# Optimization experiments

Measured on AMD Instinct MI355X. Metric: run time of the kernel, lower is better.

Reference implementation:

```python
import jax, jax.numpy as jnp
import numpy as np

B, L, H = 2, 4096, 1024
ED, N, R, K = 2048, 16, 64, 4


def setup_inputs() -> dict:
    key = jax.random.key(0)
    ks = jax.random.split(key, 8)
    w = lambda i, shape, s=0.02: jax.random.normal(ks[i], shape, jnp.float32) * s
    # dt bias initialized like Mamba: inv-softplus of dt ~ logU(1e-3, 1e-1)
    dt = jnp.exp(jax.random.uniform(ks[7], (ED,)) * (np.log(0.1) - np.log(0.001)) + np.log(0.001))
    dt = jnp.clip(dt, 1e-4)
    inv_dt = dt + jnp.log(-jnp.expm1(-dt))
    A = jnp.broadcast_to(jnp.arange(1, N + 1, dtype=jnp.float32), (ED, N))
    return dict(
        x=jax.random.normal(ks[0], (B, L, H), jnp.float32),
        in_proj_w=w(1, (2 * ED, H)),
        conv_w=w(2, (ED, K), 0.2),
        conv_b=jnp.zeros((ED,), jnp.float32),
        x_proj_w=w(3, (R + 2 * N, ED)),
        dt_w=w(4, (ED, R), 64 ** -0.5),
        dt_b=inv_dt,
        A_log=jnp.log(A),
        D=jnp.ones((ED,), jnp.float32),
        out_proj_w=w(5, (H, ED)),
    )


def reference(x, in_proj_w, conv_w, conv_b, x_proj_w, dt_w, dt_b, A_log, D, out_proj_w):
    Bq, Lq, Hq = x.shape
    EDq, Kq = conv_w.shape
    Rq = dt_w.shape[1]
    Nq = A_log.shape[1]

    # in_proj -> [B, L, 2*ED]; chunk into hidden_states and gate
    xz = jnp.einsum('blh,eh->ble', x, in_proj_w)
    hs, gate = jnp.split(xz, 2, axis=-1)

    # causal depthwise conv1d along L (padding K-1 on the left), then SiLU
    hs_pad = jnp.pad(hs, ((0, 0), (Kq - 1, 0), (0, 0)))  # [B, L+K-1, ED]
    conv = conv_b
    for k in range(Kq):  # K=4, fixed small loop
        conv = conv + hs_pad[:, k:k + Lq, :] * conv_w[:, k]
    hs = jax.nn.silu(conv)  # [B, L, ED]

    # x_proj -> split into dt (rank R), B (N), C (N)
    ssm = jnp.einsum('ble,pe->blp', hs, x_proj_w)
    dtr, Bm, Cm = jnp.split(ssm, [Rq, Rq + Nq], axis=-1)

    # dt_proj + softplus (delta_softplus=True with delta_bias)
    delta = jax.nn.softplus(jnp.einsum('blr,er->ble', dtr, dt_w) + dt_b)  # [B,L,ED]

    A = -jnp.exp(A_log)  # [ED, N]

    # selective scan: h_t = exp(delta_t*A)*h_{t-1} + delta_t*B_t*u_t ; y_t = <h_t, C_t>
    def step(h, inp):
        d_t, B_t, C_t, u_t = inp  # [B,ED], [B,N], [B,N], [B,ED]
        dA = jnp.exp(d_t[..., None] * A)                      # [B,ED,N]
        h = dA * h + (d_t * u_t)[..., None] * B_t[:, None, :]  # [B,ED,N]
        y = jnp.einsum('ben,bn->be', h, C_t)                   # [B,ED]
        return h, y

    h0 = jnp.zeros((Bq, EDq, Nq), x.dtype)
    xs = (jnp.moveaxis(delta, 1, 0), jnp.moveaxis(Bm, 1, 0),
          jnp.moveaxis(Cm, 1, 0), jnp.moveaxis(hs, 1, 0))
    _, ys = jax.lax.scan(step, h0, xs)  # ys: [L, B, ED]

    y = jnp.moveaxis(ys, 0, 1) + hs * D      # skip term D*u
    y = y * jax.nn.silu(gate)                # gated output
    return jnp.einsum('ble,he->blh', y, out_proj_w)
```

## Files before the change

### kernel.cpp

```cpp
#include <hip/hip_runtime.h>


typedef float f32x4 __attribute__((ext_vector_type(4)));
typedef short short8 __attribute__((ext_vector_type(8)));
typedef unsigned short u16;

#define DEV __device__ __forceinline__

DEV float bf2f(u16 u) {
  union { unsigned int i; float f; } v; v.i = ((unsigned int)u) << 16; return v.f;
}
DEV u16 f2bf(float f) {
  union { float f; unsigned int i; } v; v.f = f;
  return (u16)((v.i + 0x7fffu + ((v.i >> 16) & 1u)) >> 16);
}

DEV void gload_lds16(const void* g, void* l) {
  __builtin_amdgcn_global_load_lds(
      (const __attribute__((address_space(1))) unsigned int*)g,
      (__attribute__((address_space(3))) unsigned int*)l, 16, 0, 0);
}

DEV void mfma_bf16(f32x4& d, short8 a, short8 b) {
  asm("v_mfma_f32_16x16x32_bf16 %0, %1, %2, %0" : "+v"(d) : "v"(a), "v"(b));
}

template <int N> DEV void wait_vmcnt() {
  if constexpr (N == 0)      asm volatile("s_waitcnt vmcnt(0)" ::: "memory");
  else if constexpr (N == 1) asm volatile("s_waitcnt vmcnt(1)" ::: "memory");
  else if constexpr (N == 2) asm volatile("s_waitcnt vmcnt(2)" ::: "memory");
  else if constexpr (N == 4) asm volatile("s_waitcnt vmcnt(4)" ::: "memory");
  else if constexpr (N == 6) asm volatile("s_waitcnt vmcnt(6)" ::: "memory");
  else                       asm volatile("s_waitcnt vmcnt(8)" ::: "memory");
}

#define SYNC_PRE() do { __builtin_amdgcn_s_barrier(); \
  asm volatile("s_waitcnt lgkmcnt(0)" ::: "memory"); \
  __builtin_amdgcn_sched_barrier(0); \
  __builtin_amdgcn_s_setprio(1); } while (0)
#define SYNC_POST() do { __builtin_amdgcn_s_setprio(0); \
  __builtin_amdgcn_sched_barrier(0); \
  __builtin_amdgcn_s_barrier(); } while (0)

template <int EPI>
__global__ __launch_bounds__(512, 2) void gemm256_kernel(
    const u16* __restrict__ A, const u16* __restrict__ Bw,
    int M, int N, int Kd,
    float* __restrict__ o_f32, u16* __restrict__ o_b16a, u16* __restrict__ o_b16b)
{
  __shared__ u16 lds[65536];
  const int tid  = threadIdx.x;
  const int wave = tid >> 6;
  const int lane = tid & 63;
  const int row  = lane & 15;
  const int g    = lane >> 4;
  const int wr   = wave >> 2;
  const int wc   = wave & 3;

  const int nbx = N >> 8;
  const int nwg = gridDim.x;
  const int cpx = nwg >> 3;
  const int swzb = (blockIdx.x & 7) * cpx + (blockIdx.x >> 3);
  const int bx = swzb % nbx, by = swzb / nbx;
  const int rowBase = by * 256, colBase = bx * 256;

  auto STAGE = [&](int isB, int h, int kt) {
    const u16* src = isB ? Bw : A;
    const int baseRow = (isB ? colBase : rowBase) + h * 128;
    const int ldsbase = (kt & 1) * 32768 + isB * 16384 + h * 8192;
    const int kk = kt * 64;
#pragma unroll
    for (int q = 0; q < 2; ++q) {
      int c = q * 512 + tid;
      int r = c >> 3;
      int qc = (c & 7) ^ (r & 7);
      gload_lds16(src + (size_t)(baseRow + r) * Kd + kk + qc * 8,
                  (void*)(lds + ldsbase + (q * 512 + wave * 64) * 8));
    }
  };

  f32x4 acc[8][4];
#pragma unroll
  for (int i = 0; i < 8; ++i)
#pragma unroll
    for (int j = 0; j < 4; ++j) acc[i][j] = (f32x4){0.f, 0.f, 0.f, 0.f};

  short8 rA[8], rB0[4], rB1[4];

#define LDA(PAR, MH) do { \
  _Pragma("unroll") for (int mi = 0; mi < 4; ++mi) \
  _Pragma("unroll") for (int ks = 0; ks < 2; ++ks) \
    rA[mi*2+ks] = *(const short8*)(lds + (PAR)*32768 + wr*8192 \
        + ((MH)*64 + mi*16 + row)*64 + (((ks*4 + g) ^ (row & 7))*8)); \
} while (0)

#define LDB(PAR, NH, RB) do { \
  _Pragma("unroll") for (int ni = 0; ni < 2; ++ni) \
  _Pragma("unroll") for (int ks = 0; ks < 2; ++ks) \
    (RB)[ni*2+ks] = *(const short8*)(lds + (PAR)*32768 + 16384 + (wc>>1)*8192 \
        + (((wc&1)*64 + (NH)*32 + ni*16 + row)*64) + (((ks*4 + g) ^ (row & 7))*8)); \
} while (0)

#define QUAD(MH, NH, RB) do { \
  _Pragma("unroll") for (int mi = 0; mi < 4; ++mi) \
  _Pragma("unroll") for (int ni = 0; ni < 2; ++ni) \
  _Pragma("unroll") for (int ks = 0; ks < 2; ++ks) \
    mfma_bf16(acc[(MH)*4+mi][(NH)*2+ni], rA[mi*2+ks], (RB)[ni*2+ks]); \
} while (0)

  const int nkt = Kd >> 6;
  const int niters = nkt >> 1;

  STAGE(0, 0, 0); STAGE(0, 1, 0); STAGE(1, 0, 0); STAGE(1, 1, 0);
  STAGE(1, 0, 1); STAGE(1, 1, 1); STAGE(0, 0, 1);
  wait_vmcnt<6>();
  __builtin_amdgcn_s_barrier();

  for (int i = 0; i < niters; ++i) {
    const int kt0 = 2 * i, kt1 = 2 * i + 1;
    const bool pf = (i + 1 < niters);
    LDA(0, 0); LDB(0, 0, rB0); STAGE(0, 1, kt1);
    SYNC_PRE(); QUAD(0, 0, rB0); SYNC_POST();
    LDB(0, 1, rB1);
    SYNC_PRE(); QUAD(0, 1, rB1); SYNC_POST();
    LDA(0, 1);
    if (pf) { STAGE(1, 0, kt0 + 2); STAGE(1, 1, kt0 + 2); }
    SYNC_PRE(); QUAD(1, 0, rB0); SYNC_POST();
    if (pf) { STAGE(0, 0, kt0 + 2); wait_vmcnt<6>(); } else { wait_vmcnt<0>(); }
    SYNC_PRE(); QUAD(1, 1, rB1); SYNC_POST();
    LDA(1, 0); LDB(1, 0, rB0);
    if (pf) STAGE(0, 1, kt0 + 2);
    SYNC_PRE(); QUAD(0, 0, rB0); SYNC_POST();
    LDB(1, 1, rB1);
    SYNC_PRE(); QUAD(0, 1, rB1); SYNC_POST();
    LDA(1, 1);
    if (pf) { STAGE(1, 0, kt1 + 2); STAGE(1, 1, kt1 + 2); }
    SYNC_PRE(); QUAD(1, 0, rB0); SYNC_POST();
    if (pf) { STAGE(0, 0, kt1 + 2); wait_vmcnt<6>(); } else { wait_vmcnt<0>(); }
    SYNC_PRE(); QUAD(1, 1, rB1); SYNC_POST();
  }
#undef LDA
#undef LDB
#undef QUAD

#pragma unroll
  for (int mf = 0; mf < 8; ++mf) {
    const int growb = rowBase + wr * 128 + (mf >> 2) * 64 + (mf & 3) * 16 + g * 4;
#pragma unroll
    for (int nf = 0; nf < 4; ++nf) {
      const int gcol = colBase + wc * 64 + (nf >> 1) * 32 + (nf & 1) * 16 + row;
#pragma unroll
      for (int r4 = 0; r4 < 4; ++r4) {
        const int grow = growb + r4;
        float v = acc[mf][nf][r4];
        if constexpr (EPI == 0) {
          o_f32[(size_t)grow * N + gcol] = v;
        } else {
          if (gcol < 2048) o_b16a[(size_t)grow * 2048 + gcol] = f2bf(v);
          else             o_b16b[(size_t)grow * 2048 + (gcol - 2048)] = f2bf(v);
        }
      }
    }
  }
}

template <int BM, int BN, int WM, int WN, int EPI>
__global__ __launch_bounds__(256) void gemm_bt_kernel(
    const u16* __restrict__ A, const u16* __restrict__ Bw,
    int M, int N, int Kd,
    float* __restrict__ o_f32, u16* __restrict__ o_b16a,
    u16* __restrict__ o_b16b, const float* __restrict__ bias,
    float* __restrict__ oB, float* __restrict__ oC)
{
  constexpr int MFR = BM / WM / 16;
  constexpr int NFR = BN / WN / 16;
  constexpr int TA = BM * 4;
  constexpr int TB = BN * 4;
  constexpr int TILE = (BM + BN) * 32;
  constexpr int LA3 = (TA > 192) ? ((TA - 193) / 256 + 1) : 0;
  constexpr int LB3 = (TB > 192) ? ((TB - 193) / 256 + 1) : 0;
  constexpr int LPS = LA3 + LB3;
  __shared__ u16 lds[TILE * 3];

  const int tid  = threadIdx.x;
  const int wave = tid >> 6;
  const int lane = tid & 63;
  const int row  = lane & 15;
  const int g    = lane >> 4;
  const int swz  = g ^ ((row >> 1) & 3);
  const int rowBase = blockIdx.y * BM;
  const int colBase = blockIdx.x * BN;
  const int WROW = (wave / WN) * (BM / WM);
  const int WCOL = (wave % WN) * (BN / WN);

  auto stage = [&](int kt, int bufbase) {
    const int kk = kt * 32;
#pragma unroll
    for (int c0 = 0; c0 < TA; c0 += 256) {
      int ch = c0 + tid;
      if (ch < TA) {
        int r = ch >> 2;
        int gs = (ch & 3) ^ ((r >> 1) & 3);
        gload_lds16(A + (size_t)(rowBase + r) * Kd + kk + gs * 8,
                    (void*)(lds + bufbase + (c0 + wave * 64) * 8));
      }
    }
#pragma unroll
    for (int c0 = 0; c0 < TB; c0 += 256) {
      int ch = c0 + tid;
      if (ch < TB) {
        int r = ch >> 2;
        int gs = (ch & 3) ^ ((r >> 1) & 3);
        gload_lds16(Bw + (size_t)(colBase + r) * Kd + kk + gs * 8,
                    (void*)(lds + bufbase + BM * 32 + (c0 + wave * 64) * 8));
      }
    }
  };

  f32x4 acc[MFR][NFR];
#pragma unroll
  for (int i = 0; i < MFR; ++i)
#pragma unroll
    for (int j = 0; j < NFR; ++j) acc[i][j] = (f32x4){0.f, 0.f, 0.f, 0.f};

  const int nt = Kd / 32;
  stage(0, 0);
  stage(1, TILE);
  int cur = 0;
  for (int t = 0; t < nt; ++t) {
    if (t + 2 < nt) {
      int b2 = cur + 2; if (b2 >= 3) b2 -= 3;
      stage(t + 2, b2 * TILE);
      wait_vmcnt<2 * LPS>();
    } else if (t + 1 < nt) {
      wait_vmcnt<LPS>();
    } else {
      wait_vmcnt<0>();
    }
    __builtin_amdgcn_sched_barrier(0);
    __builtin_amdgcn_s_barrier();
    __builtin_amdgcn_sched_barrier(0);
    const u16* lb = lds + cur * TILE;
    short8 af[MFR], bfr[NFR];
#pragma unroll
    for (int mi = 0; mi < MFR; ++mi)
      af[mi] = *(const short8*)(lb + (WROW + mi * 16 + row) * 32 + swz * 8);
#pragma unroll
    for (int ni = 0; ni < NFR; ++ni)
      bfr[ni] = *(const short8*)(lb + BM * 32 + (WCOL + ni * 16 + row) * 32 + swz * 8);
#pragma unroll
    for (int mi = 0; mi < MFR; ++mi)
#pragma unroll
      for (int ni = 0; ni < NFR; ++ni)
        mfma_bf16(acc[mi][ni], af[mi], bfr[ni]);
    __builtin_amdgcn_sched_barrier(0);
    __builtin_amdgcn_s_barrier();
    cur += 1; if (cur >= 3) cur -= 3;
  }

#pragma unroll
  for (int mi = 0; mi < MFR; ++mi) {
#pragma unroll
    for (int ni = 0; ni < NFR; ++ni) {
      const int gcol = colBase + WCOL + ni * 16 + row;
#pragma unroll
      for (int r = 0; r < 4; ++r) {
        const int grow = rowBase + WROW + mi * 16 + g * 4 + r;
        float v = acc[mi][ni][r];
        if constexpr (EPI == 0) {
          o_f32[(size_t)grow * N + gcol] = v;
        } else if constexpr (EPI == 1) {
          if (gcol < 2048) o_b16a[(size_t)grow * 2048 + gcol] = f2bf(v);
          else             o_b16b[(size_t)grow * 2048 + (gcol - 2048)] = f2bf(v);
        } else if constexpr (EPI == 2) {
          if (gcol < 64)      o_b16a[(size_t)grow * 64 + gcol] = f2bf(v);
          else if (gcol < 80) oB[(size_t)grow * 16 + (gcol - 64)] = v;
          else                oC[(size_t)grow * 16 + (gcol - 80)] = v;
        } else {
          float x = v + bias[gcol];
          o_f32[(size_t)grow * N + gcol] = (x > 20.f) ? x : __logf(1.f + __expf(x));
        }
      }
    }
  }
}

__global__ __launch_bounds__(256) void cvt_bf16_kernel(
    const float* __restrict__ in, u16* __restrict__ out, int n8)
{
  int i = blockIdx.x * 256 + threadIdx.x;
  if (i >= n8) return;
  const float4* p = (const float4*)(in + (size_t)i * 8);
  float4 a = p[0], b = p[1];
  float v[8] = {a.x, a.y, a.z, a.w, b.x, b.y, b.z, b.w};
  unsigned o[4];
#pragma unroll
  for (int q = 0; q < 4; ++q)
    o[q] = (unsigned)f2bf(v[2 * q]) | ((unsigned)f2bf(v[2 * q + 1]) << 16);
  *(uint4*)(out + (size_t)i * 8) = make_uint4(o[0], o[1], o[2], o[3]);
}

__global__ __launch_bounds__(256) void conv_silu_kernel(
    const u16* __restrict__ hsraw, const float* __restrict__ cw,
    const float* __restrict__ cb, u16* __restrict__ hsb)
{
  int idx = blockIdx.x * 256 + threadIdx.x;
  int e0 = (idx & 255) * 8;
  int t  = (idx >> 8) & 4095;
  int b  = idx >> 20;
  float acc[8];
  float wv[4][8];
#pragma unroll
  for (int j = 0; j < 8; ++j) acc[j] = cb[e0 + j];
#pragma unroll
  for (int k = 0; k < 4; ++k)
#pragma unroll
    for (int j = 0; j < 8; ++j) wv[k][j] = cw[(e0 + j) * 4 + k];
#pragma unroll
  for (int k = 0; k < 4; ++k) {
    int tt = t - 3 + k;
    if (tt < 0) continue;
    uint4 v4 = *(const uint4*)(hsraw + ((size_t)(b * 4096 + tt)) * 2048 + e0);
    unsigned arr[4] = {v4.x, v4.y, v4.z, v4.w};
#pragma unroll
    for (int q = 0; q < 4; ++q) {
      acc[2 * q]     += wv[k][2 * q]     * bf2f((u16)(arr[q] & 0xffffu));
      acc[2 * q + 1] += wv[k][2 * q + 1] * bf2f((u16)(arr[q] >> 16));
    }
  }
  unsigned o[4];
#pragma unroll
  for (int q = 0; q < 4; ++q) {
    float a0 = acc[2 * q], a1 = acc[2 * q + 1];
    a0 = a0 / (1.f + __expf(-a0));
    a1 = a1 / (1.f + __expf(-a1));
    o[q] = (unsigned)f2bf(a0) | ((unsigned)f2bf(a1) << 16);
  }
  *(uint4*)(hsb + ((size_t)(b * 4096 + t)) * 2048 + e0) = make_uint4(o[0], o[1], o[2], o[3]);
}

__global__ __launch_bounds__(256) void scan_phase1(
    const float* __restrict__ delta, const u16* __restrict__ hsb,
    const float* __restrict__ Bb, const float* __restrict__ alog,
    float* __restrict__ h_end, float* __restrict__ Ssum)
{
  __shared__ __align__(16) float Bs[64 * 16];
  const int tid = threadIdx.x;
  const int e = blockIdx.x * 256 + tid;
  const int c = blockIdx.y;
  const int b = blockIdx.z;
  const int t0 = c * 64;
  {
    const float* src = Bb + ((size_t)(b * 4096 + t0)) * 16;
#pragma unroll
    for (int k = 0; k < 4; ++k) Bs[tid + k * 256] = src[tid + k * 256];
  }
  float An[16];
  {
    const float4* ap = (const float4*)(alog + e * 16);
#pragma unroll
    for (int q = 0; q < 4; ++q) {
      float4 v = ap[q];
      An[4*q+0] = -__expf(v.x); An[4*q+1] = -__expf(v.y);
      An[4*q+2] = -__expf(v.z); An[4*q+3] = -__expf(v.w);
    }
  }
  __syncthreads();
  float h[16];
#pragma unroll
  for (int n = 0; n < 16; ++n) h[n] = 0.f;
  float sumd = 0.f;
  size_t base = ((size_t)(b * 4096 + t0)) * 2048 + e;
  float dd = delta[base];
  float uu = bf2f(hsb[base]);
  for (int j = 0; j < 64; ++j) {
    int jn = (j < 63) ? j + 1 : 63;
    float d_nxt = delta[base + (size_t)jn * 2048];
    float u_nxt = bf2f(hsb[base + (size_t)jn * 2048]);
    const float4* Bv = (const float4*)(Bs + j * 16);
    float4 b0 = Bv[0], b1 = Bv[1], b2 = Bv[2], b3 = Bv[3];
    float Bl[16] = {b0.x,b0.y,b0.z,b0.w, b1.x,b1.y,b1.z,b1.w,
                    b2.x,b2.y,b2.z,b2.w, b3.x,b3.y,b3.z,b3.w};
    sumd += dd;
    float du = dd * uu;
#pragma unroll
    for (int n = 0; n < 16; ++n)
      h[n] = fmaf(__expf(An[n] * dd), h[n], du * Bl[n]);
    dd = d_nxt; uu = u_nxt;
  }
  float* he = h_end + (((size_t)(b * 2048 + e)) * 64 + c) * 16;
#pragma unroll
  for (int q = 0; q < 4; ++q) {
    float4 v = {h[4*q], h[4*q+1], h[4*q+2], h[4*q+3]};
    *(float4*)(he + 4 * q) = v;
  }
  Ssum[((size_t)(b * 2048 + e)) * 64 + c] = sumd;
}

__global__ __launch_bounds__(256) void scan_phase2(
    const float* __restrict__ h_end, const float* __restrict__ Ssum,
    const float* __restrict__ alog, float* __restrict__ h_start)
{
  const int tid = threadIdx.x;
  const int n = tid & 15;
  const int G = blockIdx.x * 16 + (tid >> 4);
  const int e = G & 2047;
  const float An = -__expf(alog[e * 16 + n]);
  size_t hb = (size_t)G * 64 * 16 + n;
  size_t sb = (size_t)G * 64;
  float h = 0.f;
  constexpr int PF = 8;
  float hq[PF], Sq[PF];
#pragma unroll
  for (int j = 0; j < PF; ++j) { hq[j] = h_end[hb + (size_t)j * 16]; Sq[j] = Ssum[sb + j]; }
  for (int c0 = 0; c0 < 64; c0 += PF) {
    float hn[PF], Sn[PF];
#pragma unroll
    for (int j = 0; j < PF; ++j) {
      int cn = c0 + PF + j; cn = (cn < 64) ? cn : 63;
      hn[j] = h_end[hb + (size_t)cn * 16]; Sn[j] = Ssum[sb + cn];
    }
#pragma unroll
    for (int j = 0; j < PF; ++j) {
      h_start[hb + (size_t)(c0 + j) * 16] = h;
      h = fmaf(__expf(An * Sq[j]), h, hq[j]);
    }
#pragma unroll
    for (int j = 0; j < PF; ++j) { hq[j] = hn[j]; Sq[j] = Sn[j]; }
  }
}

__global__ __launch_bounds__(256) void scan_phase3(
    const float* __restrict__ delta, const u16* __restrict__ hsb,
    const float* __restrict__ Bb, const float* __restrict__ Cb,
    const float* __restrict__ alog, const float* __restrict__ h_start,
    const float* __restrict__ Dv, u16* __restrict__ gate_y2)
{
  __shared__ __align__(16) float Bs[64 * 16];
  __shared__ __align__(16) float Cs[64 * 16];
  const int tid = threadIdx.x;
  const int e = blockIdx.x * 256 + tid;
  const int c = blockIdx.y;
  const int b = blockIdx.z;
  const int t0 = c * 64;
  {
    const float* srcB = Bb + ((size_t)(b * 4096 + t0)) * 16;
    const float* srcC = Cb + ((size_t)(b * 4096 + t0)) * 16;
#pragma unroll
    for (int k = 0; k < 4; ++k) {
      Bs[tid + k * 256] = srcB[tid + k * 256];
      Cs[tid + k * 256] = srcC[tid + k * 256];
    }
  }
  float An[16];
  {
    const float4* ap = (const float4*)(alog + e * 16);
#pragma unroll
    for (int q = 0; q < 4; ++q) {
      float4 v = ap[q];
      An[4*q+0] = -__expf(v.x); An[4*q+1] = -__expf(v.y);
      An[4*q+2] = -__expf(v.z); An[4*q+3] = -__expf(v.w);
    }
  }
  const float De = Dv[e];
  float h[16];
  {
    const float4* hp = (const float4*)(h_start + (((size_t)(b * 2048 + e)) * 64 + c) * 16);
#pragma unroll
    for (int q = 0; q < 4; ++q) {
      float4 v = hp[q];
      h[4*q+0] = v.x; h[4*q+1] = v.y; h[4*q+2] = v.z; h[4*q+3] = v.w;
    }
  }
  __syncthreads();
  size_t base = ((size_t)(b * 4096 + t0)) * 2048 + e;
  float dd = delta[base];
  float uu = bf2f(hsb[base]);
  float gg = bf2f(gate_y2[base]);
  for (int j = 0; j < 64; ++j) {
    int jn = (j < 63) ? j + 1 : 63;
    float d_nxt = delta[base + (size_t)jn * 2048];
    float u_nxt = bf2f(hsb[base + (size_t)jn * 2048]);
    float g_nxt = bf2f(gate_y2[base + (size_t)jn * 2048]);
    const float4* Bv = (const float4*)(Bs + j * 16);
    const float4* Cv = (const float4*)(Cs + j * 16);
    float4 b0 = Bv[0], b1 = Bv[1], b2 = Bv[2], b3 = Bv[3];
    float4 c0v = Cv[0], c1v = Cv[1], c2v = Cv[2], c3v = Cv[3];
    float Bl[16] = {b0.x,b0.y,b0.z,b0.w, b1.x,b1.y,b1.z,b1.w,
                    b2.x,b2.y,b2.z,b2.w, b3.x,b3.y,b3.z,b3.w};
    float Cl[16] = {c0v.x,c0v.y,c0v.z,c0v.w, c1v.x,c1v.y,c1v.z,c1v.w,
                    c2v.x,c2v.y,c2v.z,c2v.w, c3v.x,c3v.y,c3v.z,c3v.w};
    float du = dd * uu;
    float y = 0.f;
#pragma unroll
    for (int n = 0; n < 16; ++n) {
      h[n] = fmaf(__expf(An[n] * dd), h[n], du * Bl[n]);
      y = fmaf(h[n], Cl[n], y);
    }
    float val = (y + uu * De) * (gg / (1.f + __expf(-gg)));
    gate_y2[base + (size_t)j * 2048] = f2bf(val);
    dd = d_nxt; uu = u_nxt; gg = g_nxt;
  }
}

extern "C" void kernel_launch(void* const* d_in, const int* in_sizes, int n_in,
                              void* d_out, int out_size, void* d_ws, size_t ws_size,
                              hipStream_t stream)
{
  const float* x    = (const float*)d_in[0];
  const float* w1   = (const float*)d_in[1];
  const float* cw   = (const float*)d_in[2];
  const float* cb   = (const float*)d_in[3];
  const float* xp   = (const float*)d_in[4];
  const float* dtw  = (const float*)d_in[5];
  const float* dtb  = (const float*)d_in[6];
  const float* alog = (const float*)d_in[7];
  const float* Dp   = (const float*)d_in[8];
  const float* wo   = (const float*)d_in[9];
  float* out = (float*)d_out;
  char* ws = (char*)d_ws;

  const size_t o_xb    = 0;
  const size_t o_wb1   = 16777216;
  const size_t o_xpb   = 25165824;
  const size_t o_dtwb  = 25559040;
  const size_t o_wob   = 25821184;
  const size_t o_hsraw = 30015488;
  const size_t o_gate  = 63569920;
  const size_t o_hsb   = 97124352;
  const size_t o_dtrb  = 130678784;
  const size_t o_Bb    = 131727360;
  const size_t o_Cb    = 132251648;
  const size_t o_delta = 132775936;
  const size_t WS_NEED = o_delta + 67108864 + 262144;
  if (ws_size < WS_NEED) return;

  u16* xb    = (u16*)(ws + o_xb);
  u16* wb1   = (u16*)(ws + o_wb1);
  u16* xpb   = (u16*)(ws + o_xpb);
  u16* dtwb  = (u16*)(ws + o_dtwb);
  u16* wob   = (u16*)(ws + o_wob);
  u16* hsraw = (u16*)(ws + o_hsraw);
  u16* gate  = (u16*)(ws + o_gate);
  u16* hsb   = (u16*)(ws + o_hsb);
  u16* dtrb  = (u16*)(ws + o_dtrb);
  float* Bb    = (float*)(ws + o_Bb);
  float* Cb    = (float*)(ws + o_Cb);
  float* delta = (float*)(ws + o_delta);
  float* h_end   = (float*)(ws + o_xb);
  float* h_start = (float*)(ws + o_hsraw);
  float* Ssum    = (float*)(ws + o_hsraw + 16777216);

  cvt_bf16_kernel<<<4096, 256, 0, stream>>>(x,   xb,   1048576);
  cvt_bf16_kernel<<<2048, 256, 0, stream>>>(w1,  wb1,  524288);
  cvt_bf16_kernel<<<96,   256, 0, stream>>>(xp,  xpb,  24576);
  cvt_bf16_kernel<<<64,   256, 0, stream>>>(dtw, dtwb, 16384);
  cvt_bf16_kernel<<<1024, 256, 0, stream>>>(wo,  wob,  262144);

  gemm256_kernel<1><<<512, 512, 0, stream>>>(
      xb, wb1, 8192, 4096, 1024, nullptr, hsraw, gate);
  conv_silu_kernel<<<8192, 256, 0, stream>>>(hsraw, cw, cb, hsb);
  gemm_bt_kernel<32,96,2,2,2><<<dim3(1,256), 256, 0, stream>>>(
      hsb, xpb, 8192, 96, 2048, nullptr, dtrb, nullptr, nullptr, Bb, Cb);
  gemm_bt_kernel<64,64,2,2,3><<<dim3(32,128), 256, 0, stream>>>(
      dtrb, dtwb, 8192, 2048, 64, delta, nullptr, nullptr, dtb, nullptr, nullptr);

  scan_phase1<<<dim3(8, 64, 2), 256, 0, stream>>>(delta, hsb, Bb, alog, h_end, Ssum);
  scan_phase2<<<256, 256, 0, stream>>>(h_end, Ssum, alog, h_start);
  scan_phase3<<<dim3(8, 64, 2), 256, 0, stream>>>(
      delta, hsb, Bb, Cb, alog, h_start, Dp, gate);

  gemm_bt_kernel<128,128,2,2,0><<<dim3(8,64), 256, 0, stream>>>(
      gate, wob, 8192, 1024, 2048, out, nullptr, nullptr, nullptr, nullptr, nullptr);
}
```

Before: 376.5 us.

## Restructure GEMM main-loop barriers and batch weight conversion launches

The in_proj GEMM main loop drops one of the two barriers per phase and moves the LDS-count wait to the end of each phase. Global-to-LDS staging and LDS reads are reordered inside phases, and the MFMA loop order is changed so the k-step is outermost. Separately, four weight fp32-to-bf16 conversion kernels are merged into one launch to cut launch overhead. Removing the trailing barrier risks LDS read/write races if the staging order is not safe.

Measured after the change: 376.3 us. No clear change (-0.1%).

```diff
diff --git a/kernel.cpp b/kernel.cpp
--- a/kernel.cpp
+++ b/kernel.cpp
@@ -34,13 +34,12 @@
   else                       asm volatile("s_waitcnt vmcnt(8)" ::: "memory");
 }
 
-#define SYNC_PRE() do { __builtin_amdgcn_s_barrier(); \
-  asm volatile("s_waitcnt lgkmcnt(0)" ::: "memory"); \
+#define PH_PRE() do { __builtin_amdgcn_s_barrier(); \
   __builtin_amdgcn_sched_barrier(0); \
   __builtin_amdgcn_s_setprio(1); } while (0)
-#define SYNC_POST() do { __builtin_amdgcn_s_setprio(0); \
-  __builtin_amdgcn_sched_barrier(0); \
-  __builtin_amdgcn_s_barrier(); } while (0)
+#define PH_POST() do { __builtin_amdgcn_s_setprio(0); \
+  asm volatile("s_waitcnt lgkmcnt(0)" ::: "memory"); \
+  __builtin_amdgcn_sched_barrier(0); } while (0)
 
 template <int EPI>
 __global__ __launch_bounds__(512, 2) void gemm256_kernel(
@@ -102,9 +101,9 @@
 } while (0)
 
 #define QUAD(MH, NH, RB) do { \
+  _Pragma("unroll") for (int ks = 0; ks < 2; ++ks) \
   _Pragma("unroll") for (int mi = 0; mi < 4; ++mi) \
   _Pragma("unroll") for (int ni = 0; ni < 2; ++ni) \
-  _Pragma("unroll") for (int ks = 0; ks < 2; ++ks) \
     mfma_bf16(acc[(MH)*4+mi][(NH)*2+ni], rA[mi*2+ks], (RB)[ni*2+ks]); \
 } while (0)
 
@@ -114,30 +113,48 @@
   STAGE(0, 0, 0); STAGE(0, 1, 0); STAGE(1, 0, 0); STAGE(1, 1, 0);
   STAGE(1, 0, 1); STAGE(1, 1, 1); STAGE(0, 0, 1);
   wait_vmcnt<6>();
-  __builtin_amdgcn_s_barrier();
 
   for (int i = 0; i < niters; ++i) {
     const int kt0 = 2 * i, kt1 = 2 * i + 1;
     const bool pf = (i + 1 < niters);
-    LDA(0, 0); LDB(0, 0, rB0); STAGE(0, 1, kt1);
-    SYNC_PRE(); QUAD(0, 0, rB0); SYNC_POST();
+    PH_PRE();
+    STAGE(0, 1, kt1);
+    LDB(0, 0, rB0); LDA(0, 0);
+    QUAD(0, 0, rB0);
+    PH_POST();
+    PH_PRE();
     LDB(0, 1, rB1);
-    SYNC_PRE(); QUAD(0, 1, rB1); SYNC_POST();
+    QUAD(0, 1, rB1);
+    PH_POST();
+    PH_PRE();
+    if (pf) { STAGE(1, 0, kt0 + 2); STAGE(1, 1, kt0 + 2); }
     LDA(0, 1);
-    if (pf) { STAGE(1, 0, kt0 + 2); STAGE(1, 1, kt0 + 2); }
-    SYNC_PRE(); QUAD(1, 0, rB0); SYNC_POST();
-    if (pf) { STAGE(0, 0, kt0 + 2); wait_vmcnt<6>(); } else { wait_vmcnt<0>(); }
-    SYNC_PRE(); QUAD(1, 1, rB1); SYNC_POST();
-    LDA(1, 0); LDB(1, 0, rB0);
+    QUAD(1, 0, rB0);
+    PH_POST();
+    PH_PRE();
+    if (pf) STAGE(0, 0, kt0 + 2);
+    QUAD(1, 1, rB1);
+    PH_POST();
+    if (pf) wait_vmcnt<6>(); else wait_vmcnt<0>();
+    PH_PRE();
     if (pf) STAGE(0, 1, kt0 + 2);
-    SYNC_PRE(); QUAD(0, 0, rB0); SYNC_POST();
+    LDB(1, 0, rB0); LDA(1, 0);
+    QUAD(0, 0, rB0);
+    PH_POST();
+    PH_PRE();
     LDB(1, 1, rB1);
-    SYNC_PRE(); QUAD(0, 1, rB1); SYNC_POST();
+    QUAD(0, 1, rB1);
+    PH_POST();
+    PH_PRE();
+    if (pf) { STAGE(1, 0, kt1 + 2); STAGE(1, 1, kt1 + 2); }
     LDA(1, 1);
-    if (pf) { STAGE(1, 0, kt1 + 2); STAGE(1, 1, kt1 + 2); }
-    SYNC_PRE(); QUAD(1, 0, rB0); SYNC_POST();
-    if (pf) { STAGE(0, 0, kt1 + 2); wait_vmcnt<6>(); } else { wait_vmcnt<0>(); }
-    SYNC_PRE(); QUAD(1, 1, rB1); SYNC_POST();
+    QUAD(1, 0, rB0);
+    PH_POST();
+    PH_PRE();
+    if (pf) STAGE(0, 0, kt1 + 2);
+    QUAD(1, 1, rB1);
+    PH_POST();
+    if (pf) wait_vmcnt<6>(); else wait_vmcnt<0>();
   }
 #undef LDA
 #undef LDB
@@ -285,19 +302,39 @@
   }
 }
 
-__global__ __launch_bounds__(256) void cvt_bf16_kernel(
-    const float* __restrict__ in, u16* __restrict__ out, int n8)
-{
-  int i = blockIdx.x * 256 + threadIdx.x;
-  if (i >= n8) return;
-  const float4* p = (const float4*)(in + (size_t)i * 8);
+DEV void cvt8(const float* in, u16* out, int j) {
+  const float4* p = (const float4*)(in + (size_t)j * 8);
   float4 a = p[0], b = p[1];
   float v[8] = {a.x, a.y, a.z, a.w, b.x, b.y, b.z, b.w};
   unsigned o[4];
 #pragma unroll
   for (int q = 0; q < 4; ++q)
     o[q] = (unsigned)f2bf(v[2 * q]) | ((unsigned)f2bf(v[2 * q + 1]) << 16);
-  *(uint4*)(out + (size_t)i * 8) = make_uint4(o[0], o[1], o[2], o[3]);
+  *(uint4*)(out + (size_t)j * 8) = make_uint4(o[0], o[1], o[2], o[3]);
+}
+
+__global__ __launch_bounds__(256) void cvt_bf16_kernel(
+    const float* __restrict__ in, u16* __restrict__ out, int n8)
+{
+  int i = blockIdx.x * 256 + threadIdx.x;
+  if (i >= n8) return;
+  cvt8(in, out, i);
+}
+
+__global__ __launch_bounds__(256) void cvt4_kernel(
+    const float* __restrict__ a0, u16* __restrict__ o0, int n0,
+    const float* __restrict__ a1, u16* __restrict__ o1, int n1,
+    const float* __restrict__ a2, u16* __restrict__ o2, int n2,
+    const float* __restrict__ a3, u16* __restrict__ o3, int n3)
+{
+  int i = blockIdx.x * 256 + threadIdx.x;
+  if (i < n0)                { cvt8(a0, o0, i); return; }
+  i -= n0;
+  if (i < n1)                { cvt8(a1, o1, i); return; }
+  i -= n1;
+  if (i < n2)                { cvt8(a2, o2, i); return; }
+  i -= n2;
+  if (i < n3)                { cvt8(a3, o3, i); }
 }
 
 __global__ __launch_bounds__(256) void conv_silu_kernel(
@@ -551,11 +588,9 @@
   float* h_start = (float*)(ws + o_hsraw);
   float* Ssum    = (float*)(ws + o_hsraw + 16777216);
 
-  cvt_bf16_kernel<<<4096, 256, 0, stream>>>(x,   xb,   1048576);
-  cvt_bf16_kernel<<<2048, 256, 0, stream>>>(w1,  wb1,  524288);
-  cvt_bf16_kernel<<<96,   256, 0, stream>>>(xp,  xpb,  24576);
-  cvt_bf16_kernel<<<64,   256, 0, stream>>>(dtw, dtwb, 16384);
-  cvt_bf16_kernel<<<1024, 256, 0, stream>>>(wo,  wob,  262144);
+  cvt_bf16_kernel<<<4096, 256, 0, stream>>>(x, xb, 1048576);
+  cvt4_kernel<<<3232, 256, 0, stream>>>(
+      w1, wb1, 524288, xp, xpb, 24576, dtw, dtwb, 16384, wo, wob, 262144);
 
   gemm256_kernel<1><<<512, 512, 0, stream>>>(
       xb, wb1, 8192, 4096, 1024, nullptr, hsraw, gate);
```
